# Performance work log

Measured on AMD Instinct MI355X. Metric: run time of the kernel, lower is better.

The kernel has to match this reference:

```python
import jax, jax.numpy as jnp
import numpy as np

TOP_K = 2  # n_heads / k in SigmaMoE


def setup_inputs() -> dict:
    key = jax.random.key(0)
    k1, k2, k3, k4 = jax.random.split(key, 4)
    B, S, d = 4, 2048, 512
    E, H = 32, 128  # n_experts, expert_size
    # init scales mirror reset_parameters (std ~ 1/sqrt(fan_in)) so sigmoid router is unsaturated
    x = jax.random.normal(k1, (B, S, d), dtype=jnp.float32)
    expert_sel = jax.random.normal(k2, (E, d), dtype=jnp.float32) / np.sqrt(d).astype(np.float32)
    keys = jax.random.normal(k3, (E, d, H), dtype=jnp.float32) / np.sqrt(d).astype(np.float32)
    values = jax.random.normal(k4, (E, H, d), dtype=jnp.float32) / np.sqrt(E * H).astype(np.float32)
    return {"x": x, "expert_sel": expert_sel, "keys": keys, "values": values}


def reference(x, expert_sel, keys, values):
    # x: [B, S, d]; expert_sel: [E, d]; keys: [E, d, H]; values: [E, H, v]
    B, S, d = x.shape
    E = keys.shape[0]
    xt = x.reshape(-1, d)                       # [T, d] tokens
    T = xt.shape[0]

    # Router: sigmoid gate + top-k expert selection (eval mode: no dropout, no sel_hist)
    sel = jax.nn.sigmoid(xt @ expert_sel.T)     # [T, E]
    sel_val, sel_idx = jax.lax.top_k(sel, TOP_K)  # [T, K] each; combine is order-invariant

    # Sparse routing weights as dense [T, E] mask (zero for unselected experts,
    # so unselected expert compute is exactly cancelled -> same math as cvmm dispatch/combine)
    w = jnp.zeros((T, E), dtype=xt.dtype).at[jnp.arange(T)[:, None], sel_idx].add(sel_val)

    # Expert FFN: scores = relu(x @ keys[e]); out = sum_e w[t,e] * scores @ values[e]
    h = jax.nn.relu(jnp.einsum('td,edh->teh', xt, keys))   # [T, E, H]
    out = jnp.einsum('teh,te,ehv->tv', h, w, values)       # [T, v]
    return out.reshape(B, S, -1)
```

## Files before the change

### kernel.cpp

```cpp
#include <hip/hip_runtime.h>

#define TT 8192
#define DD 512
#define EE 32
#define HH 128

typedef float f32x4 __attribute__((ext_vector_type(4)));
typedef __bf16 bf16x8 __attribute__((ext_vector_type(8)));
typedef unsigned short u16x8 __attribute__((ext_vector_type(8)));

__device__ __forceinline__ unsigned short f2bf(float f) {
  unsigned int u = __builtin_bit_cast(unsigned int, f);
  u = (u + 0x7FFFu + ((u >> 16) & 1u)) >> 16;
  return (unsigned short)u;
}
__device__ __forceinline__ float bf2f(unsigned short h) {
  return __builtin_bit_cast(float, (unsigned int)h << 16);
}

#define GLD16(g, l)                                                            \
  __builtin_amdgcn_global_load_lds(                                            \
      (const __attribute__((address_space(1))) unsigned int*)(g),              \
      (__attribute__((address_space(3))) unsigned int*)(l), 16, 0, 0)

__global__ __launch_bounds__(256) void convert_kernel(
    const float* __restrict__ keys, const float* __restrict__ values,
    const float* __restrict__ esel,
    unsigned short* __restrict__ keysT, unsigned short* __restrict__ valuesT,
    unsigned short* __restrict__ eselF, int* __restrict__ cur) {
  __shared__ float tile[64][68];
  int bid = blockIdx.x;
  const int t = threadIdx.x;
  if (bid >= 1024) {
    if (bid == 1024 && t < EE) cur[t] = 0;
    int f = (bid - 1024) * 256 + t;
    int lane = f & 63;
    int rest = f >> 6;
    int half = rest & 1;
    int kt = rest >> 1;
    int term = kt % 3;
    int k = kt / 3;
    int n = half * 16 + (lane & 15);
    int col = k * 32 + (lane >> 4) * 8;
    const float* s = esel + (size_t)n * DD + col;
    unsigned short o[8];
#pragma unroll
    for (int q = 0; q < 8; q++) {
      float v = s[q];
      unsigned short hh = f2bf(v);
      float r1 = v - bf2f(hh);
      unsigned short lo = f2bf(r1);
      float r2 = r1 - bf2f(lo);
      o[q] = (term == 0) ? hh : (term == 1) ? lo : f2bf(r2);
    }
    *(u16x8*)(eselF + (size_t)f * 8) = *(const u16x8*)o;
    return;
  }
  const float* src;
  unsigned short* dst;
  int R, C, r0, c0, e;
  if (bid < 512) {
    e = bid >> 4; int sub = bid & 15;
    R = DD; C = HH; r0 = (sub >> 1) * 64; c0 = (sub & 1) * 64;
    src = keys; dst = keysT;
  } else {
    bid -= 512;
    e = bid >> 4; int sub = bid & 15;
    R = HH; C = DD; r0 = (sub & 1) * 64; c0 = (sub >> 1) * 64;
    src = values; dst = valuesT;
  }
  const int rl = t >> 2, cq = (t & 3) * 16;
  const float* s0 = src + ((size_t)e * R + r0 + rl) * C + c0 + cq;
#pragma unroll
  for (int i = 0; i < 4; i++) *(float4*)&tile[rl][cq + 4 * i] = *(const float4*)(s0 + 4 * i);
  __syncthreads();
  unsigned short* d0 = dst + ((size_t)e * C + c0 + rl) * R + r0 + cq;
#pragma unroll
  for (int i = 0; i < 4; i++) {
    ushort4 v;
    v.x = f2bf(tile[cq + 4 * i + 0][rl]);
    v.y = f2bf(tile[cq + 4 * i + 1][rl]);
    v.z = f2bf(tile[cq + 4 * i + 2][rl]);
    v.w = f2bf(tile[cq + 4 * i + 3][rl]);
    *(ushort4*)(d0 + 4 * i) = v;
  }
}

__global__ __launch_bounds__(128) void router_kernel(
    const float* __restrict__ x, const unsigned short* __restrict__ eselF,
    unsigned short* __restrict__ xb, int* __restrict__ etok,
    float* __restrict__ ew, int* __restrict__ cur) {
  __shared__ float ls[32][33];
  __shared__ int bcnt[EE], bbase[EE], bcur[EE];
  const int tid = threadIdx.x;
  const int tok0 = blockIdx.x * 32;
  const int wv = tid >> 6, lane = tid & 63;
  const int ll = lane & 15, lh = lane >> 4;
  const int row = tok0 + wv * 16 + ll;

  const float* xr = x + (size_t)row * DD + lh * 8;
  unsigned short* xbr = xb + (size_t)row * DD + lh * 8;

  f32x4 acc0, acc1;
  acc0[0] = 0.f; acc0[1] = 0.f; acc0[2] = 0.f; acc0[3] = 0.f;
  acc1 = acc0;

  for (int k = 0; k < 16; k++) {
    float4 v0 = *(const float4*)(xr + k * 32);
    float4 v1 = *(const float4*)(xr + k * 32 + 4);
    float vv[8] = {v0.x, v0.y, v0.z, v0.w, v1.x, v1.y, v1.z, v1.w};
    bf16x8 ah, al, al2;
    unsigned short hs[8];
#pragma unroll
    for (int j = 0; j < 8; j++) {
      unsigned short hh = f2bf(vv[j]);
      float r1 = vv[j] - bf2f(hh);
      unsigned short lo = f2bf(r1);
      float r2 = r1 - bf2f(lo);
      hs[j] = hh;
      ah[j] = __builtin_bit_cast(__bf16, hh);
      al[j] = __builtin_bit_cast(__bf16, lo);
      al2[j] = __builtin_bit_cast(__bf16, f2bf(r2));
    }
    *(ushort4*)(xbr + k * 32) = *(ushort4*)&hs[0];
    *(ushort4*)(xbr + k * 32 + 4) = *(ushort4*)&hs[4];

    const unsigned short* fk = eselF + (size_t)k * 6 * 512 + lane * 8;
    bf16x8 bh0 = *(const bf16x8*)(fk);
    bf16x8 bh1 = *(const bf16x8*)(fk + 512);
    bf16x8 bl0 = *(const bf16x8*)(fk + 1024);
    bf16x8 bl1 = *(const bf16x8*)(fk + 1536);
    bf16x8 bm0 = *(const bf16x8*)(fk + 2048);
    bf16x8 bm1 = *(const bf16x8*)(fk + 2560);

    acc0 = __builtin_amdgcn_mfma_f32_16x16x32_bf16(ah, bh0, acc0, 0, 0, 0);
    acc0 = __builtin_amdgcn_mfma_f32_16x16x32_bf16(ah, bl0, acc0, 0, 0, 0);
    acc0 = __builtin_amdgcn_mfma_f32_16x16x32_bf16(al, bh0, acc0, 0, 0, 0);
    acc0 = __builtin_amdgcn_mfma_f32_16x16x32_bf16(ah, bm0, acc0, 0, 0, 0);
    acc0 = __builtin_amdgcn_mfma_f32_16x16x32_bf16(al, bl0, acc0, 0, 0, 0);
    acc0 = __builtin_amdgcn_mfma_f32_16x16x32_bf16(al2, bh0, acc0, 0, 0, 0);

    acc1 = __builtin_amdgcn_mfma_f32_16x16x32_bf16(ah, bh1, acc1, 0, 0, 0);
    acc1 = __builtin_amdgcn_mfma_f32_16x16x32_bf16(ah, bl1, acc1, 0, 0, 0);
    acc1 = __builtin_amdgcn_mfma_f32_16x16x32_bf16(al, bh1, acc1, 0, 0, 0);
    acc1 = __builtin_amdgcn_mfma_f32_16x16x32_bf16(ah, bm1, acc1, 0, 0, 0);
    acc1 = __builtin_amdgcn_mfma_f32_16x16x32_bf16(al, bl1, acc1, 0, 0, 0);
    acc1 = __builtin_amdgcn_mfma_f32_16x16x32_bf16(al2, bh1, acc1, 0, 0, 0);
  }

#pragma unroll
  for (int r = 0; r < 4; r++) {
    ls[wv * 16 + lh * 4 + r][ll] = acc0[r];
    ls[wv * 16 + lh * 4 + r][16 + ll] = acc1[r];
  }
  if (tid < EE) bcnt[tid] = 0;
  __syncthreads();

  int i0 = 0, i1 = 0;
  float w0 = 0.f, w1 = 0.f;
  if (tid < 32) {
    float m0 = -3.4e38f;
#pragma unroll
    for (int e2 = 0; e2 < EE; e2++) {
      float v = ls[tid][e2];
      if (v > m0) { m0 = v; i0 = e2; }
    }
    float m1 = -3.4e38f;
    i1 = (i0 == 0) ? 1 : 0;
#pragma unroll
    for (int e2 = 0; e2 < EE; e2++) {
      float v = ls[tid][e2];
      if (e2 != i0 && v > m1) { m1 = v; i1 = e2; }
    }
    w0 = 1.f / (1.f + expf(-m0));
    w1 = 1.f / (1.f + expf(-m1));
    atomicAdd(&bcnt[i0], 1);
    atomicAdd(&bcnt[i1], 1);
  }
  __syncthreads();
  if (tid < EE) { bbase[tid] = atomicAdd(&cur[tid], bcnt[tid]); bcur[tid] = 0; }
  __syncthreads();
  if (tid < 32) {
    int t = tok0 + tid;
    int p0 = bbase[i0] + atomicAdd(&bcur[i0], 1);
    etok[(size_t)i0 * TT + p0] = t;
    ew[(size_t)i0 * TT + p0] = w0;
    int p1 = bbase[i1] + atomicAdd(&bcur[i1], 1);
    etok[(size_t)i1 * TT + p1] = t | (1 << 20);
    ew[(size_t)i1 * TT + p1] = w1;
  }
}

__global__ __launch_bounds__(512) void moe_gemm_kernel(
    const unsigned short* __restrict__ xb,
    const unsigned short* __restrict__ keysT,
    const unsigned short* __restrict__ valuesT,
    const int* __restrict__ cur,
    const int* __restrict__ etok,
    const float* __restrict__ ew,
    unsigned short* __restrict__ yb) {
  const int e = blockIdx.x;
  const int cnt = cur[e];
  const int base = blockIdx.y * 64;
  if (base >= cnt) return;

  __shared__ unsigned short stage_buf[2][8192];
  __shared__ unsigned short h_swz[8192];
  __shared__ int tok_s[64];
  __shared__ int srow_s[64];
  __shared__ float w_s[64];

  const int tid = threadIdx.x;
  const int lane = tid & 63;
  const int wv = tid >> 6;
  const int wm = wv & 3;
  const int wn = wv >> 2;
  const int ll = lane & 15, lh = lane >> 4;

  const unsigned short* kT = keysT + (size_t)e * HH * DD;
  const unsigned short* vT = valuesT + (size_t)e * DD * HH;

  auto stage_b1 = [&](int c, int b) {
#pragma unroll
    for (int i = 0; i < 2; i++) {
      int P = (i * 512 + tid) * 16;
      int n = P >> 7;
      int q = P & 127;
      const char* g = (const char*)(kT + (size_t)n * DD + c * 64) + (q ^ ((n & 7) << 4));
      char* l = (char*)stage_buf[b] + (i * 512 + (tid & ~63)) * 16;
      GLD16(g, l);
    }
  };
  auto stage_b2 = [&](int c, int b) {
#pragma unroll
    for (int i = 0; i < 2; i++) {
      int P = (i * 512 + tid) * 16;
      int r = P >> 8;
      int q = P & 255;
      const char* g = (const char*)(vT + (size_t)(c * 64 + r) * HH) + (q ^ ((r & 7) << 4));
      char* l = (char*)stage_buf[b] + (i * 512 + (tid & ~63)) * 16;
      GLD16(g, l);
    }
  };

  stage_b1(0, 0);
  if (tid < 64) {
    int i = base + tid;
    if (i < cnt) {
      int v = etok[(size_t)e * TT + i];
      int t = v & 0xFFFFF;
      tok_s[tid] = t;
      srow_s[tid] = (v >> 20) * (TT + 1) + t;
      w_s[tid] = ew[(size_t)e * TT + i];
    } else {
      tok_s[tid] = etok[(size_t)e * TT + base] & 0xFFFFF;
      srow_s[tid] = TT;
      w_s[tid] = 0.f;
    }
  }
  __syncthreads();

  const unsigned short* ap = xb + (size_t)tok_s[wm * 16 + ll] * DD;

  f32x4 acc[4];
#pragma unroll
  for (int n = 0; n < 4; n++) { acc[n][0] = 0.f; acc[n][1] = 0.f; acc[n][2] = 0.f; acc[n][3] = 0.f; }

  for (int c = 0; c < 8; c++) {
    if (c < 7) stage_b1(c + 1, (c + 1) & 1);
    else       stage_b2(0, 0);
    const char* sb = (const char*)stage_buf[c & 1];
#pragma unroll
    for (int kkl = 0; kkl < 2; kkl++) {
      bf16x8 af = *(const bf16x8*)(ap + c * 64 + kkl * 32 + lh * 8);
#pragma unroll
      for (int nt = 0; nt < 4; nt++) {
        int n = wn * 64 + nt * 16 + ll;
        int boff = n * 128 + ((kkl * 64 + lh * 16) ^ ((n & 7) << 4));
        bf16x8 bfr = *(const bf16x8*)(sb + boff);
        acc[nt] = __builtin_amdgcn_mfma_f32_16x16x32_bf16(af, bfr, acc[nt], 0, 0, 0);
      }
    }
    __syncthreads();
  }

#pragma unroll
  for (int nt = 0; nt < 4; nt++) {
#pragma unroll
    for (int r = 0; r < 4; r++) {
      int row = wm * 16 + lh * 4 + r;
      int col = wn * 64 + nt * 16 + ll;
      int off = row * 256 + ((col * 2) ^ ((row & 7) << 4));
      *(unsigned short*)((char*)h_swz + off) = f2bf(fmaxf(acc[nt][r], 0.f));
    }
  }
  __syncthreads();

  bf16x8 a2[4];
#pragma unroll
  for (int kk = 0; kk < 4; kk++) {
    int row = wm * 16 + ll;
    int off = row * 256 + ((kk * 64 + lh * 16) ^ ((row & 7) << 4));
    a2[kk] = *(const bf16x8*)((const char*)h_swz + off);
  }

  float wr[4];
#pragma unroll
  for (int r = 0; r < 4; r++) wr[r] = w_s[wm * 16 + lh * 4 + r];

  __syncthreads();
  unsigned short* y_lds = h_swz;

  for (int c = 0; c < 8; c++) {
    if (c < 7) stage_b2(c + 1, (c + 1) & 1);
    const char* sb = (const char*)stage_buf[c & 1];
#pragma unroll
    for (int ntl = 0; ntl < 2; ntl++) {
      f32x4 c2;
      c2[0] = 0.f; c2[1] = 0.f; c2[2] = 0.f; c2[3] = 0.f;
#pragma unroll
      for (int kk = 0; kk < 4; kk++) {
        int r = wn * 32 + ntl * 16 + ll;
        int boff = r * 256 + ((kk * 64 + lh * 16) ^ ((r & 7) << 4));
        bf16x8 bfr = *(const bf16x8*)(sb + boff);
        c2 = __builtin_amdgcn_mfma_f32_16x16x32_bf16(a2[kk], bfr, c2, 0, 0, 0);
      }
      int colb = wn * 32 + ntl * 16 + ll;
#pragma unroll
      for (int r = 0; r < 4; r++) {
        int row = wm * 16 + lh * 4 + r;
        int off = row * 128 + ((colb * 2) ^ ((row & 7) << 4));
        *(unsigned short*)((char*)y_lds + off) = f2bf(c2[r] * wr[r]);
      }
    }
    __syncthreads();
    {
      int rr = tid >> 3, g = tid & 7;
      int off = rr * 128 + ((g * 16) ^ ((rr & 7) << 4));
      u16x8 v = *(const u16x8*)((const char*)y_lds + off);
      *(u16x8*)(yb + (size_t)srow_s[rr] * DD + c * 64 + g * 8) = v;
    }
    __syncthreads();
  }
}

__global__ __launch_bounds__(256) void combine_kernel(const unsigned short* __restrict__ yb,
                                                      float* __restrict__ out) {
  size_t i = ((size_t)blockIdx.x * 256 + threadIdx.x) * 8;
  u16x8 a = *(const u16x8*)(yb + i);
  u16x8 b = *(const u16x8*)(yb + (size_t)(TT + 1) * DD + i);
  float4 o0, o1;
  o0.x = bf2f(a[0]) + bf2f(b[0]);
  o0.y = bf2f(a[1]) + bf2f(b[1]);
  o0.z = bf2f(a[2]) + bf2f(b[2]);
  o0.w = bf2f(a[3]) + bf2f(b[3]);
  o1.x = bf2f(a[4]) + bf2f(b[4]);
  o1.y = bf2f(a[5]) + bf2f(b[5]);
  o1.z = bf2f(a[6]) + bf2f(b[6]);
  o1.w = bf2f(a[7]) + bf2f(b[7]);
  *(float4*)(out + i) = o0;
  *(float4*)(out + i + 4) = o1;
}

extern "C" void kernel_launch(void* const* d_in, const int* in_sizes, int n_in,
                              void* d_out, int out_size, void* d_ws, size_t ws_size,
                              hipStream_t stream) {
  const float* x = (const float*)d_in[0];
  const float* esel = (const float*)d_in[1];
  const float* keys = (const float*)d_in[2];
  const float* values = (const float*)d_in[3];
  float* out = (float*)d_out;

  char* p = (char*)d_ws;
  unsigned short* xb = (unsigned short*)p;      p += (size_t)TT * DD * 2;
  unsigned short* keysT = (unsigned short*)p;   p += (size_t)EE * DD * HH * 2;
  unsigned short* valuesT = (unsigned short*)p; p += (size_t)EE * DD * HH * 2;
  unsigned short* eselF = (unsigned short*)p;   p += (size_t)6144 * 8 * 2;
  int* cur = (int*)p;                           p += 256;
  int* etok = (int*)p;                          p += (size_t)EE * TT * 4;
  float* ew = (float*)p;                        p += (size_t)EE * TT * 4;
  unsigned short* yb = (unsigned short*)p;      p += (size_t)2 * (TT + 1) * DD * 2;

  convert_kernel<<<1048, 256, 0, stream>>>(keys, values, esel, keysT, valuesT, eselF, cur);
  router_kernel<<<TT / 32, 128, 0, stream>>>(x, eselF, xb, etok, ew, cur);
  moe_gemm_kernel<<<dim3(EE, TT / 64), 512, 0, stream>>>(xb, keysT, valuesT, cur, etok, ew, yb);
  combine_kernel<<<(TT * DD / 8) / 256, 256, 0, stream>>>(yb, out);
}
```

Baseline: 56.53 us.

## Switch expert GEMMs to 32x32x16 MFMA with 128-wide K/N chunks

Reworks the per-expert GEMM kernel to use 32x32x16 bf16 MFMA tiles instead of 16x16x32, remapping the 8 waves to 2 row groups by 4 column tiles. Staging chunks grow from 64 to 128 columns with a 16-row XOR swizzle, so each GEMM phase runs 4 iterations instead of 8. A separate y_lds buffer is added for output staging. The aim is fewer barriers and LDS loads per MFMA, at the cost of roughly double the shared memory per block, which may lower occupancy.

```diff
diff --git a/kernel.cpp b/kernel.cpp
--- a/kernel.cpp
+++ b/kernel.cpp
@@ -6,6 +6,7 @@
 #define HH 128
 
 typedef float f32x4 __attribute__((ext_vector_type(4)));
+typedef float f32x16 __attribute__((ext_vector_type(16)));
 typedef __bf16 bf16x8 __attribute__((ext_vector_type(8)));
 typedef unsigned short u16x8 __attribute__((ext_vector_type(8)));
 
@@ -204,8 +205,9 @@
   const int base = blockIdx.y * 64;
   if (base >= cnt) return;
 
-  __shared__ unsigned short stage_buf[2][8192];
+  __shared__ unsigned short stage_buf[2][16384];
   __shared__ unsigned short h_swz[8192];
+  __shared__ unsigned short y_lds[16384];
   __shared__ int tok_s[64];
   __shared__ int srow_s[64];
   __shared__ float w_s[64];
@@ -213,31 +215,31 @@
   const int tid = threadIdx.x;
   const int lane = tid & 63;
   const int wv = tid >> 6;
-  const int wm = wv & 3;
-  const int wn = wv >> 2;
-  const int ll = lane & 15, lh = lane >> 4;
+  const int rg = wv & 1;
+  const int nt = wv >> 1;
+  const int l31 = lane & 31, kh = lane >> 5;
 
   const unsigned short* kT = keysT + (size_t)e * HH * DD;
   const unsigned short* vT = valuesT + (size_t)e * DD * HH;
 
   auto stage_b1 = [&](int c, int b) {
 #pragma unroll
-    for (int i = 0; i < 2; i++) {
+    for (int i = 0; i < 4; i++) {
       int P = (i * 512 + tid) * 16;
-      int n = P >> 7;
-      int q = P & 127;
-      const char* g = (const char*)(kT + (size_t)n * DD + c * 64) + (q ^ ((n & 7) << 4));
+      int n = P >> 8;
+      int q = P & 255;
+      const char* g = (const char*)(kT + (size_t)n * DD + c * 128) + (q ^ ((n & 15) << 4));
       char* l = (char*)stage_buf[b] + (i * 512 + (tid & ~63)) * 16;
       GLD16(g, l);
     }
   };
   auto stage_b2 = [&](int c, int b) {
 #pragma unroll
-    for (int i = 0; i < 2; i++) {
+    for (int i = 0; i < 4; i++) {
       int P = (i * 512 + tid) * 16;
-      int r = P >> 8;
+      int n = P >> 8;
       int q = P & 255;
-      const char* g = (const char*)(vT + (size_t)(c * 64 + r) * HH) + (q ^ ((r & 7) << 4));
+      const char* g = (const char*)(vT + (size_t)(c * 128 + n) * HH) + (q ^ ((n & 15) << 4));
       char* l = (char*)stage_buf[b] + (i * 512 + (tid & ~63)) * 16;
       GLD16(g, l);
     }
@@ -260,85 +262,78 @@
   }
   __syncthreads();
 
-  const unsigned short* ap = xb + (size_t)tok_s[wm * 16 + ll] * DD;
-
-  f32x4 acc[4];
-#pragma unroll
-  for (int n = 0; n < 4; n++) { acc[n][0] = 0.f; acc[n][1] = 0.f; acc[n][2] = 0.f; acc[n][3] = 0.f; }
-
-  for (int c = 0; c < 8; c++) {
-    if (c < 7) stage_b1(c + 1, (c + 1) & 1);
+  const unsigned short* ap = xb + (size_t)tok_s[rg * 32 + l31] * DD + kh * 8;
+
+  f32x16 acc;
+#pragma unroll
+  for (int i = 0; i < 16; i++) acc[i] = 0.f;
+
+  const int bswz = (nt * 32 + l31) * 256;
+  const int bsx = (((nt * 32 + l31) & 15) << 4);
+
+  for (int c = 0; c < 4; c++) {
+    if (c < 3) stage_b1(c + 1, (c + 1) & 1);
     else       stage_b2(0, 0);
     const char* sb = (const char*)stage_buf[c & 1];
 #pragma unroll
-    for (int kkl = 0; kkl < 2; kkl++) {
-      bf16x8 af = *(const bf16x8*)(ap + c * 64 + kkl * 32 + lh * 8);
-#pragma unroll
-      for (int nt = 0; nt < 4; nt++) {
-        int n = wn * 64 + nt * 16 + ll;
-        int boff = n * 128 + ((kkl * 64 + lh * 16) ^ ((n & 7) << 4));
-        bf16x8 bfr = *(const bf16x8*)(sb + boff);
-        acc[nt] = __builtin_amdgcn_mfma_f32_16x16x32_bf16(af, bfr, acc[nt], 0, 0, 0);
-      }
+    for (int kg = 0; kg < 8; kg++) {
+      bf16x8 af = *(const bf16x8*)(ap + c * 128 + kg * 16);
+      bf16x8 bfr = *(const bf16x8*)(sb + bswz + ((kg * 32 + kh * 16) ^ bsx));
+      acc = __builtin_amdgcn_mfma_f32_32x32x16_bf16(af, bfr, acc, 0, 0, 0);
     }
     __syncthreads();
   }
 
-#pragma unroll
-  for (int nt = 0; nt < 4; nt++) {
-#pragma unroll
-    for (int r = 0; r < 4; r++) {
-      int row = wm * 16 + lh * 4 + r;
-      int col = wn * 64 + nt * 16 + ll;
-      int off = row * 256 + ((col * 2) ^ ((row & 7) << 4));
-      *(unsigned short*)((char*)h_swz + off) = f2bf(fmaxf(acc[nt][r], 0.f));
-    }
-  }
-  __syncthreads();
-
-  bf16x8 a2[4];
-#pragma unroll
-  for (int kk = 0; kk < 4; kk++) {
-    int row = wm * 16 + ll;
-    int off = row * 256 + ((kk * 64 + lh * 16) ^ ((row & 7) << 4));
-    a2[kk] = *(const bf16x8*)((const char*)h_swz + off);
-  }
-
-  float wr[4];
-#pragma unroll
-  for (int r = 0; r < 4; r++) wr[r] = w_s[wm * 16 + lh * 4 + r];
-
-  __syncthreads();
-  unsigned short* y_lds = h_swz;
-
-  for (int c = 0; c < 8; c++) {
-    if (c < 7) stage_b2(c + 1, (c + 1) & 1);
+  {
+    int colb = (nt * 32 + l31) * 2;
+#pragma unroll
+    for (int reg = 0; reg < 16; reg++) {
+      int row = rg * 32 + (reg & 3) + 8 * (reg >> 2) + 4 * kh;
+      int off = row * 256 + (colb ^ ((row & 15) << 4));
+      *(unsigned short*)((char*)h_swz + off) = f2bf(fmaxf(acc[reg], 0.f));
+    }
+  }
+  __syncthreads();
+
+  bf16x8 a2[8];
+  {
+    int row = rg * 32 + l31;
+    int s = (row & 15) << 4;
+#pragma unroll
+    for (int kg = 0; kg < 8; kg++)
+      a2[kg] = *(const bf16x8*)((const char*)h_swz + row * 256 + ((kg * 32 + kh * 16) ^ s));
+  }
+
+  for (int c = 0; c < 4; c++) {
+    if (c < 3) stage_b2(c + 1, (c + 1) & 1);
     const char* sb = (const char*)stage_buf[c & 1];
-#pragma unroll
-    for (int ntl = 0; ntl < 2; ntl++) {
-      f32x4 c2;
-      c2[0] = 0.f; c2[1] = 0.f; c2[2] = 0.f; c2[3] = 0.f;
-#pragma unroll
-      for (int kk = 0; kk < 4; kk++) {
-        int r = wn * 32 + ntl * 16 + ll;
-        int boff = r * 256 + ((kk * 64 + lh * 16) ^ ((r & 7) << 4));
-        bf16x8 bfr = *(const bf16x8*)(sb + boff);
-        c2 = __builtin_amdgcn_mfma_f32_16x16x32_bf16(a2[kk], bfr, c2, 0, 0, 0);
-      }
-      int colb = wn * 32 + ntl * 16 + ll;
-#pragma unroll
-      for (int r = 0; r < 4; r++) {
-        int row = wm * 16 + lh * 4 + r;
-        int off = row * 128 + ((colb * 2) ^ ((row & 7) << 4));
-        *(unsigned short*)((char*)y_lds + off) = f2bf(c2[r] * wr[r]);
+    f32x16 cc;
+#pragma unroll
+    for (int i = 0; i < 16; i++) cc[i] = 0.f;
+#pragma unroll
+    for (int kg = 0; kg < 8; kg++) {
+      bf16x8 bfr = *(const bf16x8*)(sb + bswz + ((kg * 32 + kh * 16) ^ bsx));
+      cc = __builtin_amdgcn_mfma_f32_32x32x16_bf16(a2[kg], bfr, cc, 0, 0, 0);
+    }
+    {
+      int colb = (nt * 32 + l31) * 2;
+#pragma unroll
+      for (int reg = 0; reg < 16; reg++) {
+        int row = rg * 32 + (reg & 3) + 8 * (reg >> 2) + 4 * kh;
+        float w = w_s[row];
+        int off = row * 256 + (colb ^ ((row & 15) << 4));
+        *(unsigned short*)((char*)y_lds + off) = f2bf(cc[reg] * w);
       }
     }
     __syncthreads();
     {
       int rr = tid >> 3, g = tid & 7;
-      int off = rr * 128 + ((g * 16) ^ ((rr & 7) << 4));
-      u16x8 v = *(const u16x8*)((const char*)y_lds + off);
-      *(u16x8*)(yb + (size_t)srow_s[rr] * DD + c * 64 + g * 8) = v;
+      int s = (rr & 15) << 4;
+      u16x8 v0 = *(const u16x8*)((const char*)y_lds + rr * 256 + ((g * 32) ^ s));
+      u16x8 v1 = *(const u16x8*)((const char*)y_lds + rr * 256 + ((g * 32 + 16) ^ s));
+      unsigned short* yo = yb + (size_t)srow_s[rr] * DD + c * 128 + g * 16;
+      *(u16x8*)yo = v0;
+      *(u16x8*)(yo + 8) = v1;
     }
     __syncthreads();
   }
```

Measured after the change: 67.76 us. +19.9%, slower.
